# Optimization experiments

Measured on AMD Instinct MI355X. Metric: run time of the kernel, lower is better.

The kernel has to match this reference:

```python
import jax, jax.numpy as jnp
import numpy as np

N_NODES = 50000
N_EDGES = 800000
F_IN = 128
NUM_GRAPHS = 64
BN_EPS = 1e-5


def _graph_conv(x, src, dst, ew, Wl, bl, Wr, n_nodes):
    # PyG GraphConv: out = lin_l(aggr_add(x_j * w_e)) + lin_r(x)
    msg = x[src] * ew[:, None]                       # [E, F]
    agg = jax.ops.segment_sum(msg, dst, num_segments=n_nodes)  # [N, F]
    return agg @ Wl + bl + x @ Wr


def setup_inputs() -> dict:
    key = jax.random.key(0)
    ks = jax.random.split(key, 16)
    x = jax.random.normal(ks[0], (N_NODES, F_IN), dtype=jnp.float32)
    edge_index = jax.random.randint(ks[1], (2, N_EDGES), 0, N_NODES, dtype=jnp.int64)
    edge_attr = jax.random.uniform(ks[2], (N_EDGES,), dtype=jnp.float32)
    batch = jnp.sort(jax.random.randint(ks[3], (N_NODES,), 0, NUM_GRAPHS, dtype=jnp.int64))

    def lin(k, fin, fout):
        s = 1.0 / np.sqrt(fin)
        return jax.random.uniform(k, (fin, fout), jnp.float32, -s, s)

    params = {
        "Wl1": lin(ks[4], F_IN, 512), "bl1": jnp.zeros((512,), jnp.float32), "Wr1": lin(ks[5], F_IN, 512),
        "Wl2": lin(ks[6], 512, 512),  "bl2": jnp.zeros((512,), jnp.float32), "Wr2": lin(ks[7], 512, 512),
        "Wl3": lin(ks[8], 512, 256),  "bl3": jnp.zeros((256,), jnp.float32), "Wr3": lin(ks[9], 512, 256),
        "bn_gamma": jnp.ones((512,), jnp.float32), "bn_beta": jnp.zeros((512,), jnp.float32),
        "bn_mean": jnp.zeros((512,), jnp.float32),  "bn_var": jnp.ones((512,), jnp.float32),
        "W4": lin(ks[10], 256, 64), "b4": jnp.zeros((64,), jnp.float32),
        "W5": lin(ks[11], 64, 1),  "b5": jnp.zeros((1,), jnp.float32),
    }
    return {"x": x, "edge_index": edge_index, "edge_attr": edge_attr, "batch": batch, **params}


def reference(x, edge_index, edge_attr, batch,
              Wl1, bl1, Wr1, Wl2, bl2, Wr2, Wl3, bl3, Wr3,
              bn_gamma, bn_beta, bn_mean, bn_var,
              W4, b4, W5, b5):
    src, dst = edge_index[0], edge_index[1]
    n = x.shape[0]
    h = jax.nn.relu(_graph_conv(x, src, dst, edge_attr, Wl1, bl1, Wr1, n))
    h = _graph_conv(h, src, dst, edge_attr, Wl2, bl2, Wr2, n)
    # BatchNorm1d in eval mode (running stats)
    h = (h - bn_mean) * jax.lax.rsqrt(bn_var + BN_EPS) * bn_gamma + bn_beta
    h = jax.nn.relu(h)
    h = jax.nn.relu(_graph_conv(h, src, dst, edge_attr, Wl3, bl3, Wr3, n))
    # global mean pool
    sums = jax.ops.segment_sum(h, batch, num_segments=NUM_GRAPHS)           # [G, 256]
    cnts = jax.ops.segment_sum(jnp.ones((n,), h.dtype), batch, num_segments=NUM_GRAPHS)
    g = sums / jnp.maximum(cnts, 1.0)[:, None]
    # dropout is identity in eval mode
    g = jax.nn.relu(g @ W4 + b4)
    return jax.nn.relu(g @ W5 + b5)  # [G, 1]
```

## Files before the change

### kernel.cpp

```cpp
#include <hip/hip_runtime.h>

#define NN 50000
#define NE 800000
#define NG 64
#define BN_EPS 1e-5f

typedef unsigned short u16;
typedef unsigned int u32;
typedef unsigned char u8;
typedef long i64b;
struct alignas(8) us4 { u16 x, y, z, w; };
typedef float f32x4 __attribute__((ext_vector_type(4)));

__device__ inline u16 f2bf_rne(float f) {
  u32 u = __float_as_uint(f);
  return (u16)((u + 0x7fff + ((u >> 16) & 1)) >> 16);
}
__device__ inline int clampi(int v, int lo, int hi) {
  return v < lo ? lo : (v > hi ? hi : v);
}
__device__ inline void gload_lds16(const void* g, void* l) {
  __builtin_amdgcn_global_load_lds(
      (const __attribute__((address_space(1))) u32*)g,
      (__attribute__((address_space(3))) u32*)l, 16, 0, 0);
}
__device__ inline float4 fp8x4f(u32 q) {
  float4 r;
  r.x = __builtin_amdgcn_cvt_f32_fp8(q, 0);
  r.y = __builtin_amdgcn_cvt_f32_fp8(q, 1);
  r.z = __builtin_amdgcn_cvt_f32_fp8(q, 2);
  r.w = __builtin_amdgcn_cvt_f32_fp8(q, 3);
  return r;
}
__device__ inline u32 f4fp8(float a, float b, float c, float d) {
  u32 p = __builtin_amdgcn_cvt_pk_fp8_f32(a, b, 0u, false);
  return __builtin_amdgcn_cvt_pk_fp8_f32(c, d, p, true);
}
__device__ inline u8 f2fp8(float v) {
  return (u8)(__builtin_amdgcn_cvt_pk_fp8_f32(v, 0.f, 0u, false) & 0xffu);
}

__global__ void k_zero32(u32* __restrict__ p, int n) {
  int i = blockIdx.x * 256 + threadIdx.x;
  if (i < n) p[i] = 0u;
}

__global__ void k_cvt_x(const float* __restrict__ x, u8* __restrict__ xf8) {
  int i = blockIdx.x * 256 + threadIdx.x;
  if (i >= NN * 128 / 8) return;
  size_t o = (size_t)i * 8;
  float4 a = *(const float4*)(x + o);
  float4 b = *(const float4*)(x + o + 4);
  u32 p0 = f4fp8(a.x, a.y, a.z, a.w);
  u32 p1 = f4fp8(b.x, b.y, b.z, b.w);
  *(uint2*)(xf8 + o) = make_uint2(p0, p1);
}

__global__ void k_count(const int* __restrict__ dst, int* __restrict__ deg) {
  int e = blockIdx.x * 256 + threadIdx.x;
  if (e < NE) atomicAdd(&deg[clampi(dst[e], 0, NN - 1)], 1);
}

__global__ void k_scan_block(const int* __restrict__ deg, int* __restrict__ excl,
                             int* __restrict__ aux) {
  __shared__ int s[256];
  int t = threadIdx.x;
  int idx = blockIdx.x * 256 + t;
  int v = (idx < NN) ? deg[idx] : 0;
  s[t] = v;
  __syncthreads();
  for (int off = 1; off < 256; off <<= 1) {
    int x = (t >= off) ? s[t - off] : 0;
    __syncthreads();
    s[t] += x;
    __syncthreads();
  }
  if (idx < NN) excl[idx] = s[t] - v;
  if (t == 255) aux[blockIdx.x] = s[255];
}

__global__ void k_scan_aux(int* aux, int nblk) {
  __shared__ int s[256];
  int t = threadIdx.x;
  int v = (t < nblk) ? aux[t] : 0;
  s[t] = v;
  __syncthreads();
  for (int off = 1; off < 256; off <<= 1) {
    int x = (t >= off) ? s[t - off] : 0;
    __syncthreads();
    s[t] += x;
    __syncthreads();
  }
  if (t < nblk) aux[t] = s[t] - v;
}

__global__ void k_fix(int* __restrict__ rowptr, const int* __restrict__ aux,
                      int* __restrict__ cursor) {
  int idx = blockIdx.x * 256 + threadIdx.x;
  if (idx < NN) {
    int v = rowptr[idx] + aux[blockIdx.x];
    rowptr[idx] = v;
    cursor[idx] = v;
  }
  if (idx == 0) rowptr[NN] = NE;
}

__global__ void k_fill(const int* __restrict__ src, const int* __restrict__ dst,
                       const float* __restrict__ ew, int* __restrict__ cursor,
                       int* __restrict__ csr_src, float* __restrict__ csr_w) {
  int e = blockIdx.x * 256 + threadIdx.x;
  if (e < NE) {
    int d = clampi(dst[e], 0, NN - 1);
    int p = atomicAdd(&cursor[d], 1);
    p = clampi(p, 0, NE - 1);
    csr_src[p] = clampi(src[e], 0, NN - 1);
    csr_w[p] = ew[e];
  }
}

__global__ void k_wt(const float* __restrict__ Wl, const float* __restrict__ Wr,
                     int FIN, int FOUT, u8* __restrict__ t8) {
  int k = blockIdx.y * 256 + threadIdx.x;
  int n = blockIdx.x;
  int K = 2 * FIN;
  if (k >= K) return;
  float v = (k < FIN) ? Wl[(size_t)k * FOUT + n] : Wr[(size_t)(k - FIN) * FOUT + n];
  t8[(size_t)n * K + k] = f2fp8(v);
}

__global__ void k_wtn(const float* __restrict__ Wl, const float* __restrict__ Wr,
                      int Kdim, int half, u8* __restrict__ t8) {
  int k = blockIdx.y * 256 + threadIdx.x;
  int n = blockIdx.x;
  if (k >= Kdim) return;
  float v = (n < half) ? Wl[(size_t)k * half + n] : Wr[(size_t)k * half + (n - half)];
  t8[(size_t)n * Kdim + k] = f2fp8(v);
}

__global__ void k_aggf512(const u8* __restrict__ xf8, const int* __restrict__ rowptr,
                          const int* __restrict__ csr_src, const float* __restrict__ csr_w,
                          u8* __restrict__ out) {
  int n = blockIdx.x;
  int t = threadIdx.x;
  int beg = rowptr[n], end = rowptr[n + 1];
  float4 acc = {0.f, 0.f, 0.f, 0.f};
  int e = beg;
  for (; e + 2 <= end; e += 2) {
    int s0 = csr_src[e], s1 = csr_src[e + 1];
    float w0 = csr_w[e], w1 = csr_w[e + 1];
    float4 v0 = fp8x4f(*(const u32*)(xf8 + (size_t)s0 * 512 + t * 4));
    float4 v1 = fp8x4f(*(const u32*)(xf8 + (size_t)s1 * 512 + t * 4));
    acc.x += v0.x * w0 + v1.x * w1;
    acc.y += v0.y * w0 + v1.y * w1;
    acc.z += v0.z * w0 + v1.z * w1;
    acc.w += v0.w * w0 + v1.w * w1;
  }
  if (e < end) {
    int s0 = csr_src[e];
    float w0 = csr_w[e];
    float4 v0 = fp8x4f(*(const u32*)(xf8 + (size_t)s0 * 512 + t * 4));
    acc.x += v0.x * w0; acc.y += v0.y * w0;
    acc.z += v0.z * w0; acc.w += v0.w * w0;
  }
  *(u32*)(out + (size_t)n * 512 + t * 4) = f4fp8(acc.x, acc.y, acc.z, acc.w);
}

__global__ void k_aggf128(const u8* __restrict__ xf8, const int* __restrict__ rowptr,
                          const int* __restrict__ csr_src, const float* __restrict__ csr_w,
                          u8* __restrict__ out) {
  int sub = threadIdx.x >> 5;
  int lane = threadIdx.x & 31;
  int n = blockIdx.x * 2 + sub;
  if (n >= NN) return;
  int beg = rowptr[n], end = rowptr[n + 1];
  float4 acc = {0.f, 0.f, 0.f, 0.f};
  int e = beg;
  for (; e + 2 <= end; e += 2) {
    int s0 = csr_src[e], s1 = csr_src[e + 1];
    float w0 = csr_w[e], w1 = csr_w[e + 1];
    float4 v0 = fp8x4f(*(const u32*)(xf8 + (size_t)s0 * 128 + lane * 4));
    float4 v1 = fp8x4f(*(const u32*)(xf8 + (size_t)s1 * 128 + lane * 4));
    acc.x += v0.x * w0 + v1.x * w1;
    acc.y += v0.y * w0 + v1.y * w1;
    acc.z += v0.z * w0 + v1.z * w1;
    acc.w += v0.w * w0 + v1.w * w1;
  }
  if (e < end) {
    int s0 = csr_src[e];
    float w0 = csr_w[e];
    float4 v0 = fp8x4f(*(const u32*)(xf8 + (size_t)s0 * 128 + lane * 4));
    acc.x += v0.x * w0; acc.y += v0.y * w0;
    acc.z += v0.z * w0; acc.w += v0.w * w0;
  }
  *(u32*)(out + (size_t)n * 128 + lane * 4) = f4fp8(acc.x, acc.y, acc.z, acc.w);
}

template <int K, int W0, int EPI>
__global__ __launch_bounds__(256) void k_gemm(
    const u8* __restrict__ A0, const u8* __restrict__ A1,
    const u8* __restrict__ Wt, const float* __restrict__ bias,
    const float* __restrict__ gamma, const float* __restrict__ beta,
    const float* __restrict__ mean, const float* __restrict__ var,
    u8* __restrict__ O8g) {
  constexpr int FOUT = 512;
  __shared__ char LDSC[32768];
  u8* AS = (u8*)LDSC;
  u8* BS = (u8*)(LDSC + 16384);
  int tid = threadIdx.x;
  int wid = tid >> 6, l = tid & 63;
  int wr = wid >> 1, wc = wid & 1;

  int nwg = gridDim.x;
  int q8 = nwg >> 3, r8 = nwg & 7;
  int xcd = blockIdx.x & 7, idx = blockIdx.x >> 3;
  int L = (xcd < r8 ? xcd * (q8 + 1) : r8 * (q8 + 1) + (xcd - r8) * q8) + idx;
  int n0 = (L >> 2) * 128, c0 = (L & 3) * 128;

  f32x4 acc[4][4] = {};

  int srw = 32 * wid + (l >> 3);
  int sch = l & 7;

  for (int k0 = 0; k0 < K; k0 += 128) {
    __syncthreads();
    {
      const u8* s; int rs; int seg;
      if (k0 < W0) { s = A0; rs = W0; seg = k0; }
      else         { s = A1; rs = K - W0; seg = k0 - W0; }
#pragma unroll
      for (int j = 0; j < 4; ++j) {
        int r = srw + 8 * j;
        int gr = n0 + r;
        if (gr >= NN) gr = NN - 1;
        int cc = sch ^ (r & 7);
        gload_lds16(s + (size_t)gr * rs + seg + cc * 16, AS + (32 * wid + 8 * j) * 128);
      }
#pragma unroll
      for (int j = 0; j < 4; ++j) {
        int r = srw + 8 * j;
        int cc = sch ^ (r & 7);
        gload_lds16(Wt + (size_t)(c0 + r) * K + k0 + cc * 16, BS + (32 * wid + 8 * j) * 128);
      }
    }
    __syncthreads();

#pragma unroll
    for (int ks = 0; ks < 4; ++ks) {
      i64b b[4];
#pragma unroll
      for (int n = 0; n < 4; ++n) {
        int col = wc * 64 + n * 16 + (l & 15);
        int byte = (col * 128 + ks * 32 + ((l >> 4) << 3)) ^ ((col & 7) << 4);
        b[n] = *(const i64b*)((const char*)BS + byte);
      }
#pragma unroll
      for (int m = 0; m < 4; ++m) {
        int row = wr * 64 + m * 16 + (l & 15);
        int byte = (row * 128 + ks * 32 + ((l >> 4) << 3)) ^ ((row & 7) << 4);
        i64b a = *(const i64b*)((const char*)AS + byte);
#pragma unroll
        for (int n = 0; n < 4; ++n)
          acc[m][n] = __builtin_amdgcn_mfma_f32_16x16x32_fp8_fp8(a, b[n], acc[m][n], 0, 0, 0);
      }
    }
  }

  __syncthreads();
  u8* O8 = (u8*)LDSC;
#pragma unroll
  for (int n = 0; n < 4; ++n) {
    int colL = wc * 64 + n * 16 + (l & 15);
    int col = c0 + colL;
    float bs = (EPI == 2) ? 0.f : bias[col];
    float sc = 1.f, sf = 0.f;
    if (EPI == 1) {
      sc = rsqrtf(var[col] + BN_EPS) * gamma[col];
      sf = beta[col] - mean[col] * sc;
    }
#pragma unroll
    for (int m = 0; m < 4; ++m) {
      int rowL0 = wr * 64 + m * 16 + ((l >> 4) << 2);
#pragma unroll
      for (int r = 0; r < 4; ++r) {
        float v = acc[m][n][r];
        if (EPI != 2) {
          v += bs;
          if (EPI == 1) v = v * sc + sf;
          v = fmaxf(v, 0.f);
        }
        int rowL = rowL0 + r;
        int byte = (rowL * 128 + colL) ^ ((rowL & 7) << 4);
        O8[byte] = f2fp8(v);
      }
    }
  }
  __syncthreads();
#pragma unroll
  for (int i = 0; i < 4; ++i) {
    int chunk = i * 256 + tid;
    int rowL = chunk >> 3;
    int cs = (chunk & 7) * 16;
    int rr = n0 + rowL;
    if (rr < NN) {
      int byte = (rowL * 128 + cs) ^ ((rowL & 7) << 4);
      *(uint4*)(O8g + (size_t)rr * FOUT + c0 + cs) = *(const uint4*)((const char*)O8 + byte);
    }
  }
}

__global__ void k_aggcomb(const u8* __restrict__ PQ, const int* __restrict__ rowptr,
                          const int* __restrict__ csr_src, const float* __restrict__ csr_w,
                          const float* __restrict__ bl3, float* __restrict__ h3) {
  int sub = threadIdx.x >> 6;
  int lane = threadIdx.x & 63;
  int n = blockIdx.x * 2 + sub;
  if (n >= NN) return;
  int beg = rowptr[n], end = rowptr[n + 1];
  float4 acc = {0.f, 0.f, 0.f, 0.f};
  int e = beg;
  for (; e + 2 <= end; e += 2) {
    int s0 = csr_src[e], s1 = csr_src[e + 1];
    float w0 = csr_w[e], w1 = csr_w[e + 1];
    float4 v0 = fp8x4f(*(const u32*)(PQ + (size_t)s0 * 512 + lane * 4));
    float4 v1 = fp8x4f(*(const u32*)(PQ + (size_t)s1 * 512 + lane * 4));
    acc.x += v0.x * w0 + v1.x * w1;
    acc.y += v0.y * w0 + v1.y * w1;
    acc.z += v0.z * w0 + v1.z * w1;
    acc.w += v0.w * w0 + v1.w * w1;
  }
  if (e < end) {
    int s0 = csr_src[e];
    float w0 = csr_w[e];
    float4 v0 = fp8x4f(*(const u32*)(PQ + (size_t)s0 * 512 + lane * 4));
    acc.x += v0.x * w0; acc.y += v0.y * w0;
    acc.z += v0.z * w0; acc.w += v0.w * w0;
  }
  float4 qv = fp8x4f(*(const u32*)(PQ + (size_t)n * 512 + 256 + lane * 4));
  float4 bb = *(const float4*)(bl3 + lane * 4);
  float4 o;
  o.x = fmaxf(acc.x + qv.x + bb.x, 0.f);
  o.y = fmaxf(acc.y + qv.y + bb.y, 0.f);
  o.z = fmaxf(acc.z + qv.z + bb.z, 0.f);
  o.w = fmaxf(acc.w + qv.w + bb.w, 0.f);
  *(float4*)(h3 + (size_t)n * 256 + lane * 4) = o;
}

__global__ void k_counts(const int* __restrict__ batch, float* __restrict__ cnt) {
  int g = threadIdx.x;
  int lo = 0, hi = NN;
  while (lo < hi) { int m = (lo + hi) >> 1; if (batch[m] < g) lo = m + 1; else hi = m; }
  int a = lo;
  lo = 0; hi = NN;
  int g1 = g + 1;
  while (lo < hi) { int m = (lo + hi) >> 1; if (batch[m] < g1) lo = m + 1; else hi = m; }
  cnt[g] = (float)(lo - a);
}

__global__ void k_pool(const float* __restrict__ h, const int* __restrict__ batch,
                       float* __restrict__ sums) {
  int f = threadIdx.x;
  int n0 = blockIdx.x * 128;
  int n1 = n0 + 128; if (n1 > NN) n1 = NN;
  float acc = 0.f;
  int cur = clampi(batch[n0], 0, NG - 1);
  for (int n = n0; n < n1; ++n) {
    int g = clampi(batch[n], 0, NG - 1);
    if (g != cur) {
      atomicAdd(&sums[(size_t)cur * 256 + f], acc);
      acc = 0.f;
      cur = g;
    }
    acc += h[(size_t)n * 256 + f];
  }
  atomicAdd(&sums[(size_t)cur * 256 + f], acc);
}

__global__ void k_mlp(const float* __restrict__ sums, const float* __restrict__ cnt,
                      const float* __restrict__ W4, const float* __restrict__ b4,
                      const float* __restrict__ W5, const float* __restrict__ b5,
                      float* __restrict__ out) {
  __shared__ float g[256];
  int b = blockIdx.x, t = threadIdx.x;
  float inv = 1.f / fmaxf(cnt[b], 1.f);
#pragma unroll
  for (int q = 0; q < 4; ++q) g[q * 64 + t] = sums[(size_t)b * 256 + q * 64 + t] * inv;
  __syncthreads();
  float acc = 0.f;
#pragma unroll 8
  for (int k = 0; k < 256; ++k) acc += g[k] * W4[k * 64 + t];
  float a = fmaxf(acc + b4[t], 0.f) * W5[t];
  for (int off = 32; off; off >>= 1) a += __shfl_down(a, off, 64);
  if (t == 0) out[b] = fmaxf(a + b5[0], 0.f);
}

extern "C" void kernel_launch(void* const* d_in, const int* in_sizes, int n_in,
                              void* d_out, int out_size, void* d_ws, size_t ws_size,
                              hipStream_t stream) {
  const float* x     = (const float*)d_in[0];
  const int*   eidx  = (const int*)d_in[1];
  const float* ew    = (const float*)d_in[2];
  const int*   batch = (const int*)d_in[3];
  const float* Wl1 = (const float*)d_in[4];
  const float* bl1 = (const float*)d_in[5];
  const float* Wr1 = (const float*)d_in[6];
  const float* Wl2 = (const float*)d_in[7];
  const float* bl2 = (const float*)d_in[8];
  const float* Wr2 = (const float*)d_in[9];
  const float* Wl3 = (const float*)d_in[10];
  const float* bl3 = (const float*)d_in[11];
  const float* Wr3 = (const float*)d_in[12];
  const float* gamma = (const float*)d_in[13];
  const float* beta  = (const float*)d_in[14];
  const float* mean  = (const float*)d_in[15];
  const float* var   = (const float*)d_in[16];
  const float* W4 = (const float*)d_in[17];
  const float* b4 = (const float*)d_in[18];
  const float* W5 = (const float*)d_in[19];
  const float* b5 = (const float*)d_in[20];

  const int* src = eidx;
  const int* dst = eidx + NE;

  const size_t P8 = (size_t)NN * 512;
  char* w = (char*)d_ws;
  u8*  X1f8 = (u8*)w; w += P8;
  u8*  X2f8 = (u8*)w; w += P8;
  u8*  Agf8 = (u8*)w; w += P8;
  u8*  Xf8  = (u8*)w; w += (size_t)NN * 128;
  float* h3 = (float*)w; w += (size_t)NN * 256 * 4;
  u8* Wt1 = (u8*)w; w += (size_t)512 * 256;
  u8* Wt2 = (u8*)w; w += (size_t)512 * 1024;
  u8* Wt3 = (u8*)w; w += (size_t)512 * 512;
  int*   csr_src = (int*)w;   w += (size_t)NE * 4;
  float* csr_w   = (float*)w; w += (size_t)NE * 4;
  int*   rowptr  = (int*)w;   w += ((size_t)NN + 4) * 4;
  int*   cursor  = (int*)w;   w += (size_t)NN * 4;
  int*   aux     = (int*)w;   w += 1024;
  float* sums    = (float*)w; w += (size_t)NG * 256 * 4;
  float* cnt     = (float*)w; w += 1024;

  int nblk = (NN + 255) / 256;

  k_zero32<<<nblk, 256, 0, stream>>>((u32*)cursor, NN);
  k_count<<<(NE + 255) / 256, 256, 0, stream>>>(dst, cursor);
  k_scan_block<<<nblk, 256, 0, stream>>>(cursor, rowptr, aux);
  k_scan_aux<<<1, 256, 0, stream>>>(aux, nblk);
  k_fix<<<nblk, 256, 0, stream>>>(rowptr, aux, cursor);
  k_fill<<<(NE + 255) / 256, 256, 0, stream>>>(src, dst, ew, cursor, csr_src, csr_w);
  k_cvt_x<<<(NN * 128 / 8 + 255) / 256, 256, 0, stream>>>(x, Xf8);
  k_wt<<<dim3(512, 1), 256, 0, stream>>>(Wl1, Wr1, 128, 512, Wt1);
  k_wt<<<dim3(512, 4), 256, 0, stream>>>(Wl2, Wr2, 512, 512, Wt2);
  k_wtn<<<dim3(512, 2), 256, 0, stream>>>(Wl3, Wr3, 512, 256, Wt3);

  const int NWG = 391 * 4;

  k_aggf128<<<(NN + 1) / 2, 64, 0, stream>>>(Xf8, rowptr, csr_src, csr_w, Agf8);
  k_gemm<256, 128, 0><<<NWG, 256, 0, stream>>>(
      Agf8, Xf8, Wt1, bl1, nullptr, nullptr, nullptr, nullptr, X1f8);

  k_aggf512<<<NN, 128, 0, stream>>>(X1f8, rowptr, csr_src, csr_w, Agf8);
  k_gemm<1024, 512, 1><<<NWG, 256, 0, stream>>>(
      Agf8, X1f8, Wt2, bl2, gamma, beta, mean, var, X2f8);

  k_gemm<512, 512, 2><<<NWG, 256, 0, stream>>>(
      X2f8, X2f8, Wt3, nullptr, nullptr, nullptr, nullptr, nullptr, Agf8);
  k_aggcomb<<<(NN + 1) / 2, 128, 0, stream>>>(Agf8, rowptr, csr_src, csr_w, bl3, h3);

  k_zero32<<<(NG * 256 + 255) / 256, 256, 0, stream>>>((u32*)sums, NG * 256);
  k_pool<<<(NN + 127) / 128, 256, 0, stream>>>(h3, batch, sums);
  k_counts<<<1, 64, 0, stream>>>(batch, cnt);
  k_mlp<<<NG, 64, 0, stream>>>(sums, cnt, W4, b4, W5, b5, (float*)d_out);
}
```

Measured before the change: 429.2 us.

## Split gather-aggregation kernels into 64-byte feature slices across 16-node blocks

The three CSR gather kernels now give each 16-lane group one node and one 64-byte slice of its features. Each 256-thread block covers 16 nodes, and consecutive block indices cover the different feature slices of the same node group. Before, one block or half-wave handled a whole feature row for one or two nodes. The aim is to raise per-wave parallelism and memory-level parallelism by letting one wave process four nodes at once, and to give the cache a chance to serve the slices of the same source rows. The cost is that edge indices and weights are loaded once per slice, and each gathered segment is only 64 bytes.

```diff
diff --git a/kernel.cpp b/kernel.cpp
--- a/kernel.cpp
+++ b/kernel.cpp
@@ -12,10 +12,6 @@
 struct alignas(8) us4 { u16 x, y, z, w; };
 typedef float f32x4 __attribute__((ext_vector_type(4)));
 
-__device__ inline u16 f2bf_rne(float f) {
-  u32 u = __float_as_uint(f);
-  return (u16)((u + 0x7fff + ((u >> 16) & 1)) >> 16);
-}
 __device__ inline int clampi(int v, int lo, int hi) {
   return v < lo ? lo : (v > hi ? hi : v);
 }
@@ -140,16 +136,18 @@
 __global__ void k_aggf512(const u8* __restrict__ xf8, const int* __restrict__ rowptr,
                           const int* __restrict__ csr_src, const float* __restrict__ csr_w,
                           u8* __restrict__ out) {
-  int n = blockIdx.x;
-  int t = threadIdx.x;
-  int beg = rowptr[n], end = rowptr[n + 1];
+  int slice = blockIdx.x & 7;
+  int node = (blockIdx.x >> 3) * 16 + (threadIdx.x >> 4);
+  if (node >= NN) return;
+  int cb = slice * 64 + (threadIdx.x & 15) * 4;
+  int beg = rowptr[node], end = rowptr[node + 1];
   float4 acc = {0.f, 0.f, 0.f, 0.f};
   int e = beg;
   for (; e + 2 <= end; e += 2) {
     int s0 = csr_src[e], s1 = csr_src[e + 1];
     float w0 = csr_w[e], w1 = csr_w[e + 1];
-    float4 v0 = fp8x4f(*(const u32*)(xf8 + (size_t)s0 * 512 + t * 4));
-    float4 v1 = fp8x4f(*(const u32*)(xf8 + (size_t)s1 * 512 + t * 4));
+    float4 v0 = fp8x4f(*(const u32*)(xf8 + (size_t)s0 * 512 + cb));
+    float4 v1 = fp8x4f(*(const u32*)(xf8 + (size_t)s1 * 512 + cb));
     acc.x += v0.x * w0 + v1.x * w1;
     acc.y += v0.y * w0 + v1.y * w1;
     acc.z += v0.z * w0 + v1.z * w1;
@@ -158,28 +156,28 @@
   if (e < end) {
     int s0 = csr_src[e];
     float w0 = csr_w[e];
-    float4 v0 = fp8x4f(*(const u32*)(xf8 + (size_t)s0 * 512 + t * 4));
+    float4 v0 = fp8x4f(*(const u32*)(xf8 + (size_t)s0 * 512 + cb));
     acc.x += v0.x * w0; acc.y += v0.y * w0;
     acc.z += v0.z * w0; acc.w += v0.w * w0;
   }
-  *(u32*)(out + (size_t)n * 512 + t * 4) = f4fp8(acc.x, acc.y, acc.z, acc.w);
+  *(u32*)(out + (size_t)node * 512 + cb) = f4fp8(acc.x, acc.y, acc.z, acc.w);
 }
 
 __global__ void k_aggf128(const u8* __restrict__ xf8, const int* __restrict__ rowptr,
                           const int* __restrict__ csr_src, const float* __restrict__ csr_w,
                           u8* __restrict__ out) {
-  int sub = threadIdx.x >> 5;
-  int lane = threadIdx.x & 31;
-  int n = blockIdx.x * 2 + sub;
-  if (n >= NN) return;
-  int beg = rowptr[n], end = rowptr[n + 1];
+  int slice = blockIdx.x & 1;
+  int node = (blockIdx.x >> 1) * 16 + (threadIdx.x >> 4);
+  if (node >= NN) return;
+  int cb = slice * 64 + (threadIdx.x & 15) * 4;
+  int beg = rowptr[node], end = rowptr[node + 1];
   float4 acc = {0.f, 0.f, 0.f, 0.f};
   int e = beg;
   for (; e + 2 <= end; e += 2) {
     int s0 = csr_src[e], s1 = csr_src[e + 1];
     float w0 = csr_w[e], w1 = csr_w[e + 1];
-    float4 v0 = fp8x4f(*(const u32*)(xf8 + (size_t)s0 * 128 + lane * 4));
-    float4 v1 = fp8x4f(*(const u32*)(xf8 + (size_t)s1 * 128 + lane * 4));
+    float4 v0 = fp8x4f(*(const u32*)(xf8 + (size_t)s0 * 128 + cb));
+    float4 v1 = fp8x4f(*(const u32*)(xf8 + (size_t)s1 * 128 + cb));
     acc.x += v0.x * w0 + v1.x * w1;
     acc.y += v0.y * w0 + v1.y * w1;
     acc.z += v0.z * w0 + v1.z * w1;
@@ -188,11 +186,48 @@
   if (e < end) {
     int s0 = csr_src[e];
     float w0 = csr_w[e];
-    float4 v0 = fp8x4f(*(const u32*)(xf8 + (size_t)s0 * 128 + lane * 4));
+    float4 v0 = fp8x4f(*(const u32*)(xf8 + (size_t)s0 * 128 + cb));
     acc.x += v0.x * w0; acc.y += v0.y * w0;
     acc.z += v0.z * w0; acc.w += v0.w * w0;
   }
-  *(u32*)(out + (size_t)n * 128 + lane * 4) = f4fp8(acc.x, acc.y, acc.z, acc.w);
+  *(u32*)(out + (size_t)node * 128 + cb) = f4fp8(acc.x, acc.y, acc.z, acc.w);
+}
+
+__global__ void k_aggcomb(const u8* __restrict__ PQ, const int* __restrict__ rowptr,
+                          const int* __restrict__ csr_src, const float* __restrict__ csr_w,
+                          const float* __restrict__ bl3, float* __restrict__ h3) {
+  int slice = blockIdx.x & 3;
+  int node = (blockIdx.x >> 2) * 16 + (threadIdx.x >> 4);
+  if (node >= NN) return;
+  int cb = slice * 64 + (threadIdx.x & 15) * 4;
+  int beg = rowptr[node], end = rowptr[node + 1];
+  float4 acc = {0.f, 0.f, 0.f, 0.f};
+  int e = beg;
+  for (; e + 2 <= end; e += 2) {
+    int s0 = csr_src[e], s1 = csr_src[e + 1];
+    float w0 = csr_w[e], w1 = csr_w[e + 1];
+    float4 v0 = fp8x4f(*(const u32*)(PQ + (size_t)s0 * 512 + cb));
+    float4 v1 = fp8x4f(*(const u32*)(PQ + (size_t)s1 * 512 + cb));
+    acc.x += v0.x * w0 + v1.x * w1;
+    acc.y += v0.y * w0 + v1.y * w1;
+    acc.z += v0.z * w0 + v1.z * w1;
+    acc.w += v0.w * w0 + v1.w * w1;
+  }
+  if (e < end) {
+    int s0 = csr_src[e];
+    float w0 = csr_w[e];
+    float4 v0 = fp8x4f(*(const u32*)(PQ + (size_t)s0 * 512 + cb));
+    acc.x += v0.x * w0; acc.y += v0.y * w0;
+    acc.z += v0.z * w0; acc.w += v0.w * w0;
+  }
+  float4 qv = fp8x4f(*(const u32*)(PQ + (size_t)node * 512 + 256 + cb));
+  float4 bb = *(const float4*)(bl3 + cb);
+  float4 o;
+  o.x = fmaxf(acc.x + qv.x + bb.x, 0.f);
+  o.y = fmaxf(acc.y + qv.y + bb.y, 0.f);
+  o.z = fmaxf(acc.z + qv.z + bb.z, 0.f);
+  o.w = fmaxf(acc.w + qv.w + bb.w, 0.f);
+  *(float4*)(h3 + (size_t)node * 256 + cb) = o;
 }
 
 template <int K, int W0, int EPI>
@@ -306,43 +341,6 @@
       *(uint4*)(O8g + (size_t)rr * FOUT + c0 + cs) = *(const uint4*)((const char*)O8 + byte);
     }
   }
-}
-
-__global__ void k_aggcomb(const u8* __restrict__ PQ, const int* __restrict__ rowptr,
-                          const int* __restrict__ csr_src, const float* __restrict__ csr_w,
-                          const float* __restrict__ bl3, float* __restrict__ h3) {
-  int sub = threadIdx.x >> 6;
-  int lane = threadIdx.x & 63;
-  int n = blockIdx.x * 2 + sub;
-  if (n >= NN) return;
-  int beg = rowptr[n], end = rowptr[n + 1];
-  float4 acc = {0.f, 0.f, 0.f, 0.f};
-  int e = beg;
-  for (; e + 2 <= end; e += 2) {
-    int s0 = csr_src[e], s1 = csr_src[e + 1];
-    float w0 = csr_w[e], w1 = csr_w[e + 1];
-    float4 v0 = fp8x4f(*(const u32*)(PQ + (size_t)s0 * 512 + lane * 4));
-    float4 v1 = fp8x4f(*(const u32*)(PQ + (size_t)s1 * 512 + lane * 4));
-    acc.x += v0.x * w0 + v1.x * w1;
-    acc.y += v0.y * w0 + v1.y * w1;
-    acc.z += v0.z * w0 + v1.z * w1;
-    acc.w += v0.w * w0 + v1.w * w1;
-  }
-  if (e < end) {
-    int s0 = csr_src[e];
-    float w0 = csr_w[e];
-    float4 v0 = fp8x4f(*(const u32*)(PQ + (size_t)s0 * 512 + lane * 4));
-    acc.x += v0.x * w0; acc.y += v0.y * w0;
-    acc.z += v0.z * w0; acc.w += v0.w * w0;
-  }
-  float4 qv = fp8x4f(*(const u32*)(PQ + (size_t)n * 512 + 256 + lane * 4));
-  float4 bb = *(const float4*)(bl3 + lane * 4);
-  float4 o;
-  o.x = fmaxf(acc.x + qv.x + bb.x, 0.f);
-  o.y = fmaxf(acc.y + qv.y + bb.y, 0.f);
-  o.z = fmaxf(acc.z + qv.z + bb.z, 0.f);
-  o.w = fmaxf(acc.w + qv.w + bb.w, 0.f);
-  *(float4*)(h3 + (size_t)n * 256 + lane * 4) = o;
 }
 
 __global__ void k_counts(const int* __restrict__ batch, float* __restrict__ cnt) {
@@ -440,6 +438,7 @@
   float* cnt     = (float*)w; w += 1024;
 
   int nblk = (NN + 255) / 256;
+  int ngrp = (NN + 15) / 16;
 
   k_zero32<<<nblk, 256, 0, stream>>>((u32*)cursor, NN);
   k_count<<<(NE + 255) / 256, 256, 0, stream>>>(dst, cursor);
@@ -454,17 +453,17 @@
 
   const int NWG = 391 * 4;
 
-  k_aggf128<<<(NN + 1) / 2, 64, 0, stream>>>(Xf8, rowptr, csr_src, csr_w, Agf8);
+  k_aggf128<<<ngrp * 2, 256, 0, stream>>>(Xf8, rowptr, csr_src, csr_w, Agf8);
   k_gemm<256, 128, 0><<<NWG, 256, 0, stream>>>(
       Agf8, Xf8, Wt1, bl1, nullptr, nullptr, nullptr, nullptr, X1f8);
 
-  k_aggf512<<<NN, 128, 0, stream>>>(X1f8, rowptr, csr_src, csr_w, Agf8);
+  k_aggf512<<<ngrp * 8, 256, 0, stream>>>(X1f8, rowptr, csr_src, csr_w, Agf8);
   k_gemm<1024, 512, 1><<<NWG, 256, 0, stream>>>(
       Agf8, X1f8, Wt2, bl2, gamma, beta, mean, var, X2f8);
 
   k_gemm<512, 512, 2><<<NWG, 256, 0, stream>>>(
       X2f8, X2f8, Wt3, nullptr, nullptr, nullptr, nullptr, nullptr, Agf8);
-  k_aggcomb<<<(NN + 1) / 2, 128, 0, stream>>>(Agf8, rowptr, csr_src, csr_w, bl3, h3);
+  k_aggcomb<<<ngrp * 4, 256, 0, stream>>>(Agf8, rowptr, csr_src, csr_w, bl3, h3);
 
   k_zero32<<<(NG * 256 + 255) / 256, 256, 0, stream>>>((u32*)sums, NG * 256);
   k_pool<<<(NN + 127) / 128, 256, 0, stream>>>(h3, batch, sums);
```

Result: slower. 503.9 us (+17.4%).
